# Performance work log

Hardware: AMD Instinct MI355X
Metric: run time of the kernel (lower is better)

Reference implementation:

```python
import jax, jax.numpy as jnp
import numpy as np

N = 10000        # num nodes
E = 640000       # num edges
FIN = 128        # input feature dim
NH = 8           # num heads
FOUT = 16        # out features per head (NH*FOUT == FIN)
NEG_SLOPE = 0.2
EPS = 1e-16


def setup_inputs() -> dict:
    key = jax.random.key(0)
    ks = jax.random.split(key, 7)
    x = jax.random.normal(ks[0], (N, FIN), dtype=jnp.float32)
    edges = jax.random.randint(ks[1], (2, E), 0, N, dtype=jnp.int64)
    # kaiming-uniform-ish init scale
    s = float(np.sqrt(6.0 / FIN))
    W_proj = jax.random.uniform(ks[2], (NH * FOUT, FIN), minval=-s, maxval=s, dtype=jnp.float32)
    W_skip = jax.random.uniform(ks[3], (NH * FOUT, FIN), minval=-s, maxval=s, dtype=jnp.float32)
    sf = float(np.sqrt(6.0 / FOUT))
    score_src = jax.random.uniform(ks[4], (1, NH, FOUT), minval=-sf, maxval=sf, dtype=jnp.float32)
    score_tgt = jax.random.uniform(ks[5], (1, NH, FOUT), minval=-sf, maxval=sf, dtype=jnp.float32)
    bias = jnp.zeros((NH * FOUT,), dtype=jnp.float32)
    return {"x": x, "edges": edges, "W_proj": W_proj, "W_skip": W_skip,
            "score_src": score_src, "score_tgt": score_tgt, "bias": bias}


def reference(x, edges, W_proj, W_skip, score_src, score_tgt, bias):
    src, tgt = edges[0], edges[1]
    # project: [N, NH, FOUT]
    proj = (x @ W_proj.T).reshape(N, NH, FOUT)
    # per-node scores: [N, NH]
    s_src = (proj * score_src).sum(-1)
    s_tgt = (proj * score_tgt).sum(-1)
    # lift to edges and score: [E, NH]
    scores = jax.nn.leaky_relu(s_src[src] + s_tgt[tgt], negative_slope=NEG_SLOPE)
    # neighborhood-aware softmax (global max subtraction, as in original)
    exp_scores = jnp.exp(scores - jnp.max(scores))
    denom = jax.ops.segment_sum(exp_scores, tgt, num_segments=N)  # [N, NH]
    att = exp_scores / (denom[tgt] + EPS)                          # [E, NH]
    # weighted aggregation: [N, NH, FOUT]
    weighted = proj[src] * att[:, :, None]
    out = jax.ops.segment_sum(weighted, tgt, num_segments=N)
    # skip connection (dims differ per-head, so skip_proj is used), concat, bias
    out = out + (x @ W_skip.T).reshape(N, NH, FOUT)
    out = out.reshape(N, NH * FOUT) + bias
    return out
```

## Files before the change

kernel.cpp:

```cpp
#include <hip/hip_runtime.h>
#include <hip/hip_bf16.h>

#define FIN   128
#define NH    8
#define NEG   0.2f
#define HB    256
#define NMAX  10240
#define RSW   (NMAX / 2)

typedef __attribute__((ext_vector_type(8))) short short8;
typedef __attribute__((ext_vector_type(4))) float f32x4;

__device__ __forceinline__ short f2bf(float f) {
    unsigned u = __float_as_uint(f);
    return (short)((u + 0x7FFFu + ((u >> 16) & 1u)) >> 16);
}
__device__ __forceinline__ float bflo(unsigned p) { return __uint_as_float(p << 16); }
__device__ __forceinline__ float bfhi(unsigned p) { return __uint_as_float(p & 0xFFFF0000u); }
__device__ __forceinline__ float ld_f(const void* p, int i, bool bf16) {
    if (bf16) {
        unsigned h = ((const unsigned short*)p)[i];
        return __uint_as_float(h << 16);
    }
    return ((const float*)p)[i];
}
__device__ __forceinline__ short8 ld_frag(const void* p, size_t off, bool bf16) {
    if (bf16) return *(const short8*)((const short*)p + off);
    const float* f = (const float*)p + off;
    f32x4 f0 = *(const f32x4*)f;
    f32x4 f1 = *(const f32x4*)(f + 4);
    short8 r;
    r[0] = f2bf(f0[0]); r[1] = f2bf(f0[1]); r[2] = f2bf(f0[2]); r[3] = f2bf(f0[3]);
    r[4] = f2bf(f1[0]); r[5] = f2bf(f1[1]); r[6] = f2bf(f1[2]); r[7] = f2bf(f1[3]);
    return r;
}
__device__ __forceinline__ float escore(float ss, float st) {
    float v = ss + st;
    v = v > 0.f ? v : NEG * v;
    return __expf(fminf(v, 60.f));
}
__device__ __forceinline__ bool wave_bf16(const unsigned* x32) {
    unsigned w  = x32[threadIdx.x & 63];
    unsigned ex = (w >> 7) & 0xFFu;
    return __popcll(__ballot(ex >= 118u && ex <= 130u)) >= 48;
}
__device__ __forceinline__ bool wave_e64(const int* e32) {
    return __popcll(__ballot(e32[2 * (threadIdx.x & 63) + 1] == 0)) == 64;
}

__global__ __launch_bounds__(512) void k_hist(
    const int* __restrict__ e32, unsigned* __restrict__ hist2w,
    int N, int E, int perB)
{
    __shared__ unsigned l32[RSW];
    const bool e64 = wave_e64(e32);
    const int b = blockIdx.x, t = threadIdx.x;
    const int nw = (N + 1) >> 1;
    for (int j = t; j < nw; j += 512) l32[j] = 0;
    __syncthreads();
    const int lo = b * perB;
    const int hi = min(lo + perB, E);
    int te[5];
#pragma unroll
    for (int k = 0; k < 5; ++k) {
        int i = lo + t + k * 512;
        te[k] = -1;
        if (i < hi)
            te[k] = e64 ? ((const int2*)e32)[(size_t)E + i].x : e32[(size_t)E + i];
    }
#pragma unroll
    for (int k = 0; k < 5; ++k)
        if (te[k] >= 0)
            atomicAdd(&l32[te[k] >> 1], 1u << ((te[k] & 1) << 4));
    for (int i = lo + t + 5 * 512; i < hi; i += 512) {
        int tg = e64 ? ((const int2*)e32)[(size_t)E + i].x : e32[(size_t)E + i];
        atomicAdd(&l32[tg >> 1], 1u << ((tg & 1) << 4));
    }
    __syncthreads();
    const int nw4 = (nw + 3) >> 2;
    uint4* dst = (uint4*)(hist2w + (size_t)b * RSW);
    const uint4* src = (const uint4*)l32;
    for (int j = t; j < nw4; j += 512) dst[j] = src[j];
}

__global__ __launch_bounds__(256) void k_gemmscan(
    const void* __restrict__ x, const void* __restrict__ Wp,
    const void* __restrict__ Ws,
    const void* __restrict__ ssrcw, const void* __restrict__ stgtw,
    unsigned short* __restrict__ projb, unsigned short* __restrict__ skipb,
    float* __restrict__ s_src, float* __restrict__ s_tgt,
    const unsigned* __restrict__ hist2w, unsigned* __restrict__ pbase2w,
    unsigned* __restrict__ cnt2w,
    int N, int tiles, int halfTiles, int csBlocks)
{
    if ((int)blockIdx.x < csBlocks) {
        const int j = blockIdx.x * 256 + threadIdx.x;
        if (j >= RSW) return;
        const int nw = (N + 1) >> 1;
        if (j >= nw) { cnt2w[j] = 0; return; }
        unsigned s0 = 0, s1 = 0;
#pragma unroll 8
        for (int r = 0; r < HB; ++r) {
            unsigned v = hist2w[(size_t)r * RSW + j];
            pbase2w[(size_t)r * RSW + j] = s0 | (s1 << 16);
            s0 += v & 0xFFFFu;
            s1 += v >> 16;
        }
        cnt2w[j] = s0 | (s1 << 16);
        return;
    }
    const int wt = ((int)blockIdx.x - csBlocks) * 4 + ((int)threadIdx.x >> 6);
    if (wt >= tiles) return;
    const bool bf16 = wave_bf16((const unsigned*)x);
    const int lane = threadIdx.x & 63;
    const int mat = (wt >= halfTiles) ? 1 : 0;
    const int m0 = (mat ? wt - halfTiles : wt) * 16;
    const int mr = lane & 15;
    const int kb = lane >> 4;

    short8 a[4];
    const size_t xoff = (size_t)(m0 + mr) * FIN + kb * 8;
#pragma unroll
    for (int s = 0; s < 4; ++s) a[s] = ld_frag(x, xoff + s * 32, bf16);

    const void* W = mat ? Ws : Wp;
    f32x4 acc[8];
#pragma unroll
    for (int c = 0; c < 8; ++c) {
        acc[c] = (f32x4){0.f, 0.f, 0.f, 0.f};
        const size_t woff = (size_t)(c * 16 + mr) * FIN + kb * 8;
#pragma unroll
        for (int s = 0; s < 4; ++s) {
            short8 b = ld_frag(W, woff + s * 32, bf16);
            acc[c] = __builtin_amdgcn_mfma_f32_16x16x32_bf16(a[s], b, acc[c], 0, 0, 0);
        }
    }
    if (mat == 0) {
#pragma unroll
        for (int c = 0; c < 8; ++c) {
            float sw = ld_f(ssrcw, c * 16 + mr, bf16);
            float tw = ld_f(stgtw, c * 16 + mr, bf16);
#pragma unroll
            for (int r = 0; r < 4; ++r) {
                int row = m0 + kb * 4 + r;
                float v = acc[c][r];
                projb[(size_t)row * FIN + c * 16 + mr] = (unsigned short)f2bf(v);
                float vs = v * sw, vt = v * tw;
#pragma unroll
                for (int o = 8; o >= 1; o >>= 1) {
                    vs += __shfl_xor(vs, o);
                    vt += __shfl_xor(vt, o);
                }
                if (mr == 0) {
                    s_src[row * NH + c] = vs;
                    s_tgt[row * NH + c] = vt;
                }
            }
        }
    } else {
#pragma unroll
        for (int c = 0; c < 8; ++c)
#pragma unroll
            for (int r = 0; r < 4; ++r)
                skipb[(size_t)(m0 + kb * 4 + r) * FIN + c * 16 + mr] =
                    (unsigned short)f2bf(acc[c][r]);
    }
}

__global__ __launch_bounds__(256) void k_place(
    const int* __restrict__ e32, const unsigned* __restrict__ cnt2w,
    const unsigned* __restrict__ pbase2w, int* __restrict__ offs,
    int* __restrict__ sorted_src, int N, int E, int perB)
{
    __shared__ int cur[NMAX];
    __shared__ int sd[256];
    const bool e64 = wave_e64(e32);
    const int b = blockIdx.x, t = threadIdx.x;

    {
        const uint4* c4 = (const uint4*)cnt2w + t * 5;
        uint4 v[5];
        int sum = 0;
#pragma unroll
        for (int q = 0; q < 5; ++q) {
            v[q] = c4[q];
            sum += (int)((v[q].x & 0xFFFFu) + (v[q].x >> 16))
                 + (int)((v[q].y & 0xFFFFu) + (v[q].y >> 16))
                 + (int)((v[q].z & 0xFFFFu) + (v[q].z >> 16))
                 + (int)((v[q].w & 0xFFFFu) + (v[q].w >> 16));
        }
        sd[t] = sum;
        __syncthreads();
#pragma unroll
        for (int off = 1; off < 256; off <<= 1) {
            int add = (t >= off) ? sd[t - off] : 0;
            __syncthreads();
            sd[t] += add;
            __syncthreads();
        }
        int run = sd[t] - sum;
        const uint4* pb4 = (const uint4*)(pbase2w + (size_t)b * RSW) + t * 5;
        const int base = t * 40;
#pragma unroll
        for (int q = 0; q < 5; ++q) {
            uint4 pb = pb4[q];
            unsigned cw[4] = {v[q].x, v[q].y, v[q].z, v[q].w};
            unsigned pw[4] = {pb.x, pb.y, pb.z, pb.w};
#pragma unroll
            for (int u = 0; u < 4; ++u) {
                int idx = base + q * 8 + u * 2;
                int c0 = (int)(cw[u] & 0xFFFFu), c1 = (int)(cw[u] >> 16);
                cur[idx] = run + (int)(pw[u] & 0xFFFFu);
                if (b == 0 && idx < N) offs[idx] = run;
                run += c0;
                cur[idx + 1] = run + (int)(pw[u] >> 16);
                if (b == 0 && idx + 1 < N) offs[idx + 1] = run;
                run += c1;
            }
        }
        if (b == 0 && t == 255) offs[N] = run;
    }
    __syncthreads();

    const int lo = b * perB;
    const int hi = min(lo + perB, E);
    int se[10], te[10];
#pragma unroll
    for (int k = 0; k < 10; ++k) {
        int i = lo + t + k * 256;
        te[k] = -1;
        if (i < hi) {
            if (e64) {
                se[k] = ((const int2*)e32)[(size_t)i].x;
                te[k] = ((const int2*)e32)[(size_t)E + i].x;
            } else {
                se[k] = e32[i];
                te[k] = e32[(size_t)E + i];
            }
        }
    }
#pragma unroll
    for (int k = 0; k < 10; ++k) {
        if (te[k] >= 0) {
            int pos = atomicAdd(&cur[te[k]], 1);
            sorted_src[pos] = se[k];
        }
    }
    for (int i = lo + t + 10 * 256; i < hi; i += 256) {
        int s, tg;
        if (e64) { s = ((const int2*)e32)[(size_t)i].x; tg = ((const int2*)e32)[(size_t)E + i].x; }
        else     { s = e32[i];                           tg = e32[(size_t)E + i]; }
        int pos = atomicAdd(&cur[tg], 1);
        sorted_src[pos] = s;
    }
}

__global__ __launch_bounds__(256) void k_aggregate(
    const int* __restrict__ offs, const int* __restrict__ sorted_src,
    const float* __restrict__ s_src, const float* __restrict__ s_tgt,
    const unsigned short* __restrict__ projb, const unsigned short* __restrict__ skipb,
    const void* __restrict__ bias, void* __restrict__ out,
    const unsigned* __restrict__ x32, int N)
{
    const bool bf16 = wave_bf16(x32);
    const int n = blockIdx.x * 4 + ((int)threadIdx.x >> 6);
    if (n >= N) return;
    const int l = threadIdx.x & 63;
    const int start = offs[n], end = offs[n + 1];
    const int h = l >> 3;
    const int c2 = l * 2;
    const float st = s_tgt[(size_t)n * NH + h];

    float ae[8], ao[8], d[8];
#pragma unroll
    for (int k = 0; k < 8; ++k) { ae[k] = 0.f; ao[k] = 0.f; d[k] = 0.f; }

    const int cnt8 = (end - start) >> 3;
    int e = start;
    if (cnt8 > 0) {
        int idx[8];
#pragma unroll
        for (int k = 0; k < 8; ++k) idx[k] = sorted_src[e + k];
        for (int g = 0; g < cnt8; ++g) {
            int cu[8];
#pragma unroll
            for (int k = 0; k < 8; ++k) cu[k] = idx[k];
            e += 8;
            if (g + 1 < cnt8) {
#pragma unroll
                for (int k = 0; k < 8; ++k) idx[k] = sorted_src[e + k];
            }
            unsigned p[8];
#pragma unroll
            for (int k = 0; k < 8; ++k)
                p[k] = *(const unsigned*)(projb + (size_t)cu[k] * FIN + c2);
            float w[8];
#pragma unroll
            for (int k = 0; k < 8; ++k)
                w[k] = escore(s_src[(size_t)cu[k] * NH + h], st);
#pragma unroll
            for (int k = 0; k < 8; ++k) {
                ae[k] += w[k] * bflo(p[k]);
                ao[k] += w[k] * bfhi(p[k]);
                d[k]  += w[k];
            }
        }
    }
    for (; e < end; ++e) {
        int s = sorted_src[e];
        float w = escore(s_src[(size_t)s * NH + h], st);
        unsigned p = *(const unsigned*)(projb + (size_t)s * FIN + c2);
        ae[0] += w * bflo(p); ao[0] += w * bfhi(p); d[0] += w;
    }

    float num_e = ((ae[0] + ae[1]) + (ae[2] + ae[3])) + ((ae[4] + ae[5]) + (ae[6] + ae[7]));
    float num_o = ((ao[0] + ao[1]) + (ao[2] + ao[3])) + ((ao[4] + ao[5]) + (ao[6] + ao[7]));
    float den   = ((d[0] + d[1]) + (d[2] + d[3])) + ((d[4] + d[5]) + (d[6] + d[7]));
    float inv = 1.f / (den + 1e-16f);
    unsigned skp = *(const unsigned*)(skipb + (size_t)n * FIN + c2);
    float be, bo;
    if (bf16) {
        unsigned bb = *(const unsigned*)((const unsigned short*)bias + c2);
        be = bflo(bb); bo = bfhi(bb);
    } else {
        float2 b2 = *(const float2*)((const float*)bias + c2);
        be = b2.x; bo = b2.y;
    }
    float oe = num_e * inv + bflo(skp) + be;
    float oo = num_o * inv + bfhi(skp) + bo;
    if (bf16) {
        unsigned pr = ((unsigned)(unsigned short)f2bf(oo) << 16)
                    | (unsigned)(unsigned short)f2bf(oe);
        ((unsigned*)out)[((size_t)n * FIN + c2) >> 1] = pr;
    } else {
        float2 o2; o2.x = oe; o2.y = oo;
        *(float2*)((float*)out + (size_t)n * FIN + c2) = o2;
    }
}

extern "C" void kernel_launch(void* const* d_in, const int* in_sizes, int n_in,
                              void* d_out, int out_size, void* d_ws, size_t ws_size,
                              hipStream_t stream)
{
    const void* x    = d_in[0];
    const int* edges = (const int*)d_in[1];
    const void* Wp   = d_in[2];
    const void* Ws   = d_in[3];
    const void* ssw  = d_in[4];
    const void* stw  = d_in[5];
    const void* bias = d_in[6];

    const int N = in_sizes[0] / FIN;
    const int E = in_sizes[1] / 2;

    char* wp = (char*)d_ws;
    auto takeB = [&wp](size_t bytes) {
        char* p = wp;
        wp += (bytes + 255) & ~(size_t)255;
        return p;
    };
    unsigned short* projb = (unsigned short*)takeB((size_t)N * FIN * 2);
    unsigned short* skipb = (unsigned short*)takeB((size_t)N * FIN * 2);
    float* s_src      = (float*)takeB((size_t)N * NH * 4);
    float* s_tgt      = (float*)takeB((size_t)N * NH * 4);
    int* sorted_src   = (int*)takeB((size_t)E * 4);
    int* offs         = (int*)takeB((size_t)(N + 8) * 4);
    unsigned* cnt2w   = (unsigned*)takeB((size_t)RSW * 4);
    unsigned* hist2w  = (unsigned*)takeB((size_t)HB * RSW * 4);
    unsigned* pbase2w = (unsigned*)takeB((size_t)HB * RSW * 4);

    const int halfTiles = (N + 15) / 16;
    const int tiles     = 2 * halfTiles;
    const int gemmBlks  = (tiles + 3) / 4;
    const int csBlocks  = (RSW + 255) / 256;
    const int perB      = (E + HB - 1) / HB;

    k_hist<<<HB, 512, 0, stream>>>(edges, hist2w, N, E, perB);
    k_gemmscan<<<csBlocks + gemmBlks, 256, 0, stream>>>(
        x, Wp, Ws, ssw, stw, projb, skipb, s_src, s_tgt,
        hist2w, pbase2w, cnt2w, N, tiles, halfTiles, csBlocks);
    k_place<<<HB, 256, 0, stream>>>(edges, cnt2w, pbase2w, offs, sorted_src, N, E, perB);
    k_aggregate<<<(N + 3) / 4, 256, 0, stream>>>(offs, sorted_src, s_src, s_tgt, projb,
                                                 skipb, bias, d_out, (const unsigned*)x, N);
}
```

Measured before the change: 136.7 us.

## Pad CSR segments to multiples of eight with a dummy node and vectorize edge loads

Each target's edge segment in the sorted CSR is padded to a multiple of eight and the gaps are filled with a sentinel node index N. Node N gets a zero projection row and an s_src of -1e30, so its attention weight comes out as zero. This removes the scalar tail loop in aggregation and lets indices be read with aligned int4 loads. The histogram and placement kernels now read edge pairs as vector loads, which cuts load instructions. The trade-off is extra padded work and memory, and correctness depends on escore mapping -1e30 to zero weight.

```diff
diff --git a/kernel.cpp b/kernel.cpp
--- a/kernel.cpp
+++ b/kernel.cpp
@@ -60,22 +60,34 @@
     __syncthreads();
     const int lo = b * perB;
     const int hi = min(lo + perB, E);
-    int te[5];
-#pragma unroll
-    for (int k = 0; k < 5; ++k) {
-        int i = lo + t + k * 512;
-        te[k] = -1;
-        if (i < hi)
-            te[k] = e64 ? ((const int2*)e32)[(size_t)E + i].x : e32[(size_t)E + i];
-    }
-#pragma unroll
-    for (int k = 0; k < 5; ++k)
-        if (te[k] >= 0)
-            atomicAdd(&l32[te[k] >> 1], 1u << ((te[k] & 1) << 4));
-    for (int i = lo + t + 5 * 512; i < hi; i += 512) {
-        int tg = e64 ? ((const int2*)e32)[(size_t)E + i].x : e32[(size_t)E + i];
-        atomicAdd(&l32[tg >> 1], 1u << ((tg & 1) << 4));
-    }
+    const int pairs = (hi - lo) >> 1;
+    int ta[6], tb[6];
+#pragma unroll
+    for (int k = 0; k < 3; ++k) {
+        int p = t + k * 512;
+        ta[k] = -1;
+        if (p < pairs) {
+            int i = lo + 2 * p;
+            if (e64) {
+                int4 v = *(const int4*)(e32 + 2 * ((size_t)E + i));
+                ta[k] = v.x; tb[k] = v.z;
+            } else {
+                int2 v = *(const int2*)(e32 + (size_t)E + i);
+                ta[k] = v.x; tb[k] = v.y;
+            }
+        }
+    }
+#pragma unroll
+    for (int k = 0; k < 3; ++k)
+        if (ta[k] >= 0) {
+            atomicAdd(&l32[ta[k] >> 1], 1u << ((ta[k] & 1) << 4));
+            atomicAdd(&l32[tb[k] >> 1], 1u << ((tb[k] & 1) << 4));
+        }
+    if (t == 0)
+        for (int i = lo + 2 * pairs; i < hi; ++i) {
+            int tg = e64 ? ((const int2*)e32)[(size_t)E + i].x : e32[(size_t)E + i];
+            atomicAdd(&l32[tg >> 1], 1u << ((tg & 1) << 4));
+        }
     __syncthreads();
     const int nw4 = (nw + 3) >> 2;
     uint4* dst = (uint4*)(hist2w + (size_t)b * RSW);
@@ -94,6 +106,10 @@
     int N, int tiles, int halfTiles, int csBlocks)
 {
     if ((int)blockIdx.x < csBlocks) {
+        if (blockIdx.x == 0) {
+            if (threadIdx.x < FIN) projb[(size_t)N * FIN + threadIdx.x] = 0;
+            if (threadIdx.x < NH)  s_src[(size_t)N * NH + threadIdx.x] = -1e30f;
+        }
         const int j = blockIdx.x * 256 + threadIdx.x;
         if (j >= RSW) return;
         const int nw = (N + 1) >> 1;
@@ -184,10 +200,10 @@
 #pragma unroll
         for (int q = 0; q < 5; ++q) {
             v[q] = c4[q];
-            sum += (int)((v[q].x & 0xFFFFu) + (v[q].x >> 16))
-                 + (int)((v[q].y & 0xFFFFu) + (v[q].y >> 16))
-                 + (int)((v[q].z & 0xFFFFu) + (v[q].z >> 16))
-                 + (int)((v[q].w & 0xFFFFu) + (v[q].w >> 16));
+            sum += (int)(((v[q].x & 0xFFFFu) + 7u) & ~7u) + (int)(((v[q].x >> 16) + 7u) & ~7u)
+                 + (int)(((v[q].y & 0xFFFFu) + 7u) & ~7u) + (int)(((v[q].y >> 16) + 7u) & ~7u)
+                 + (int)(((v[q].z & 0xFFFFu) + 7u) & ~7u) + (int)(((v[q].z >> 16) + 7u) & ~7u)
+                 + (int)(((v[q].w & 0xFFFFu) + 7u) & ~7u) + (int)(((v[q].w >> 16) + 7u) & ~7u);
         }
         sd[t] = sum;
         __syncthreads();
@@ -209,13 +225,19 @@
 #pragma unroll
             for (int u = 0; u < 4; ++u) {
                 int idx = base + q * 8 + u * 2;
-                int c0 = (int)(cw[u] & 0xFFFFu), c1 = (int)(cw[u] >> 16);
-                cur[idx] = run + (int)(pw[u] & 0xFFFFu);
-                if (b == 0 && idx < N) offs[idx] = run;
-                run += c0;
-                cur[idx + 1] = run + (int)(pw[u] >> 16);
-                if (b == 0 && idx + 1 < N) offs[idx + 1] = run;
-                run += c1;
+#pragma unroll
+                for (int half = 0; half < 2; ++half) {
+                    int c  = (int)((cw[u] >> (half * 16)) & 0xFFFFu);
+                    int pbv = (int)((pw[u] >> (half * 16)) & 0xFFFFu);
+                    int cp = (c + 7) & ~7;
+                    cur[idx + half] = run + pbv;
+                    if (b == 0) {
+                        if (idx + half < N) offs[idx + half] = run;
+                        for (int hgap = c; hgap < cp; ++hgap)
+                            sorted_src[run + hgap] = N;
+                    }
+                    run += cp;
+                }
             }
         }
         if (b == 0 && t == 255) offs[N] = run;
@@ -224,35 +246,41 @@
 
     const int lo = b * perB;
     const int hi = min(lo + perB, E);
-    int se[10], te[10];
-#pragma unroll
-    for (int k = 0; k < 10; ++k) {
-        int i = lo + t + k * 256;
-        te[k] = -1;
-        if (i < hi) {
+    const int pairs = (hi - lo) >> 1;
+    int sa[5], sb[5], ta[5], tb[5];
+#pragma unroll
+    for (int k = 0; k < 5; ++k) {
+        int p = t + k * 256;
+        ta[k] = -1;
+        if (p < pairs) {
+            int i = lo + 2 * p;
             if (e64) {
-                se[k] = ((const int2*)e32)[(size_t)i].x;
-                te[k] = ((const int2*)e32)[(size_t)E + i].x;
+                int4 sv = *(const int4*)(e32 + 2 * (size_t)i);
+                int4 tv = *(const int4*)(e32 + 2 * ((size_t)E + i));
+                sa[k] = sv.x; sb[k] = sv.z; ta[k] = tv.x; tb[k] = tv.z;
             } else {
-                se[k] = e32[i];
-                te[k] = e32[(size_t)E + i];
-            }
-        }
-    }
-#pragma unroll
-    for (int k = 0; k < 10; ++k) {
-        if (te[k] >= 0) {
-            int pos = atomicAdd(&cur[te[k]], 1);
-            sorted_src[pos] = se[k];
-        }
-    }
-    for (int i = lo + t + 10 * 256; i < hi; i += 256) {
-        int s, tg;
-        if (e64) { s = ((const int2*)e32)[(size_t)i].x; tg = ((const int2*)e32)[(size_t)E + i].x; }
-        else     { s = e32[i];                           tg = e32[(size_t)E + i]; }
-        int pos = atomicAdd(&cur[tg], 1);
-        sorted_src[pos] = s;
-    }
+                int2 sv = *(const int2*)(e32 + (size_t)i);
+                int2 tv = *(const int2*)(e32 + (size_t)E + i);
+                sa[k] = sv.x; sb[k] = sv.y; ta[k] = tv.x; tb[k] = tv.y;
+            }
+        }
+    }
+#pragma unroll
+    for (int k = 0; k < 5; ++k) {
+        if (ta[k] >= 0) {
+            int p0 = atomicAdd(&cur[ta[k]], 1);
+            sorted_src[p0] = sa[k];
+            int p1 = atomicAdd(&cur[tb[k]], 1);
+            sorted_src[p1] = sb[k];
+        }
+    }
+    if (t == 0)
+        for (int i = lo + 2 * pairs; i < hi; ++i) {
+            int s, tg;
+            if (e64) { s = ((const int2*)e32)[(size_t)i].x; tg = ((const int2*)e32)[(size_t)E + i].x; }
+            else     { s = e32[i];                           tg = e32[(size_t)E + i]; }
+            sorted_src[atomicAdd(&cur[tg], 1)] = s;
+        }
 }
 
 __global__ __launch_bounds__(256) void k_aggregate(
@@ -278,17 +306,14 @@
     const int cnt8 = (end - start) >> 3;
     int e = start;
     if (cnt8 > 0) {
-        int idx[8];
-#pragma unroll
-        for (int k = 0; k < 8; ++k) idx[k] = sorted_src[e + k];
+        int4 ia = *(const int4*)(sorted_src + e);
+        int4 ib = *(const int4*)(sorted_src + e + 4);
         for (int g = 0; g < cnt8; ++g) {
-            int cu[8];
-#pragma unroll
-            for (int k = 0; k < 8; ++k) cu[k] = idx[k];
+            const int cu[8] = {ia.x, ia.y, ia.z, ia.w, ib.x, ib.y, ib.z, ib.w};
             e += 8;
             if (g + 1 < cnt8) {
-#pragma unroll
-                for (int k = 0; k < 8; ++k) idx[k] = sorted_src[e + k];
+                ia = *(const int4*)(sorted_src + e);
+                ib = *(const int4*)(sorted_src + e + 4);
             }
             unsigned p[8];
 #pragma unroll
@@ -305,12 +330,6 @@
                 d[k]  += w[k];
             }
         }
-    }
-    for (; e < end; ++e) {
-        int s = sorted_src[e];
-        float w = escore(s_src[(size_t)s * NH + h], st);
-        unsigned p = *(const unsigned*)(projb + (size_t)s * FIN + c2);
-        ae[0] += w * bflo(p); ao[0] += w * bfhi(p); d[0] += w;
     }
 
     float num_e = ((ae[0] + ae[1]) + (ae[2] + ae[3])) + ((ae[4] + ae[5]) + (ae[6] + ae[7]));
@@ -359,11 +378,11 @@
         wp += (bytes + 255) & ~(size_t)255;
         return p;
     };
-    unsigned short* projb = (unsigned short*)takeB((size_t)N * FIN * 2);
+    unsigned short* projb = (unsigned short*)takeB((size_t)(N + 1) * FIN * 2);
     unsigned short* skipb = (unsigned short*)takeB((size_t)N * FIN * 2);
-    float* s_src      = (float*)takeB((size_t)N * NH * 4);
+    float* s_src      = (float*)takeB((size_t)(N + 1) * NH * 4);
     float* s_tgt      = (float*)takeB((size_t)N * NH * 4);
-    int* sorted_src   = (int*)takeB((size_t)E * 4);
+    int* sorted_src   = (int*)takeB(((size_t)E + 8 * N) * 4);
     int* offs         = (int*)takeB((size_t)(N + 8) * 4);
     unsigned* cnt2w   = (unsigned*)takeB((size_t)RSW * 4);
     unsigned* hist2w  = (unsigned*)takeB((size_t)HB * RSW * 4);
```

After: 157.1 us. +14.9%, slower.
